# Performance work log

Hardware: AMD Instinct MI355X
Metric: run time of the kernel (lower is better)

Reference implementation:

```python
import jax, jax.numpy as jnp
import numpy as np

NV = 20000; NC = 20000; E = 500000
IN_SHAPE = 2; PE_DIM = 8; HID = 64; NL = 3
EPS = 1e-7  # GENConv message eps


def _lin(x, w, b):
    return x @ w + b


def _encode(x, pe, ew, eb, pw1, pb1, pw2, pb2):
    # relu(cat([Linear(x), 0.5*(pe_mlp(pe)+pe_mlp(-pe))], dim=1))
    def pe_mlp(p):
        return _lin(jax.nn.relu(_lin(p, pw1, pb1)), pw2, pb2)
    h = jnp.concatenate([_lin(x, ew, eb), 0.5 * (pe_mlp(pe) + pe_mlp(-pe))], axis=1)
    return jax.nn.relu(h)


def _genconv(x_src, x_dst, src, dst, ewt, lew, leb, w1, b1, w2, b2, n_dst):
    # GENConv(aggr='softmax', t=1, norm=None, msg_norm=False, edge_dim=1)
    msg = jax.nn.relu(x_src[src] + _lin(ewt, lew, leb)) + EPS  # [E, HID]
    m = jax.ops.segment_max(msg, dst, num_segments=n_dst)      # stable segment softmax
    ex = jnp.exp(msg - m[dst])
    s = jax.ops.segment_sum(ex, dst, num_segments=n_dst)
    agg = jax.ops.segment_sum(ex / (s[dst] + 1e-16) * msg, dst, num_segments=n_dst)
    out = agg + x_dst
    return _lin(jax.nn.relu(_lin(out, w1, b1)), w2, b2)  # MLP [hid -> 2hid -> hid]


def setup_inputs() -> dict:
    key = jax.random.key(0)
    ks = iter(jax.random.split(key, 64))
    d = {}
    d['x_vals'] = jax.random.normal(next(ks), (NV, IN_SHAPE), jnp.float32)
    d['x_cons'] = jax.random.normal(next(ks), (NC, IN_SHAPE), jnp.float32)
    d['pe_vals'] = jax.random.normal(next(ks), (NV, PE_DIM), jnp.float32)
    d['pe_cons'] = jax.random.normal(next(ks), (NC, PE_DIM), jnp.float32)
    d['edge_index_v2c'] = jnp.stack([
        jax.random.randint(next(ks), (E,), 0, NV),
        jax.random.randint(next(ks), (E,), 0, NC)])
    d['edge_index_c2v'] = jnp.stack([
        jax.random.randint(next(ks), (E,), 0, NC),
        jax.random.randint(next(ks), (E,), 0, NV)])
    d['edge_weight_v2c'] = jax.random.normal(next(ks), (E, 1), jnp.float32)
    d['edge_weight_c2v'] = jax.random.normal(next(ks), (E, 1), jnp.float32)
    def p(shape):
        return jax.random.normal(next(ks), shape, jnp.float32) * 0.05
    for k_ in ['vals', 'cons']:
        d[f'enc_{k_}_w'] = p((IN_SHAPE, HID // 2)); d[f'enc_{k_}_b'] = p((HID // 2,))
        d[f'pe_{k_}_w1'] = p((PE_DIM, HID)); d[f'pe_{k_}_b1'] = p((HID,))
        d[f'pe_{k_}_w2'] = p((HID, HID // 2)); d[f'pe_{k_}_b2'] = p((HID // 2,))
    for c in ['v2c', 'c2v']:
        d[f'{c}_edge_w'] = p((NL, 1, HID)); d[f'{c}_edge_b'] = p((NL, HID))
        d[f'{c}_w1'] = p((NL, HID, 2 * HID)); d[f'{c}_b1'] = p((NL, 2 * HID))
        d[f'{c}_w2'] = p((NL, 2 * HID, HID)); d[f'{c}_b2'] = p((NL, HID))
    for k_ in ['vals', 'cons']:
        d[f'pred_{k_}_w1'] = p((HID, HID)); d[f'pred_{k_}_b1'] = p((HID,))
        d[f'pred_{k_}_w2'] = p((HID, 1)); d[f'pred_{k_}_b2'] = p((1,))
    return d


def reference(x_vals, x_cons, pe_vals, pe_cons, edge_index_v2c, edge_index_c2v,
              edge_weight_v2c, edge_weight_c2v,
              enc_vals_w, enc_vals_b, pe_vals_w1, pe_vals_b1, pe_vals_w2, pe_vals_b2,
              enc_cons_w, enc_cons_b, pe_cons_w1, pe_cons_b1, pe_cons_w2, pe_cons_b2,
              v2c_edge_w, v2c_edge_b, v2c_w1, v2c_b1, v2c_w2, v2c_b2,
              c2v_edge_w, c2v_edge_b, c2v_w1, c2v_b1, c2v_w2, c2v_b2,
              pred_vals_w1, pred_vals_b1, pred_vals_w2, pred_vals_b2,
              pred_cons_w1, pred_cons_b1, pred_cons_w2, pred_cons_b2):
    vals = _encode(x_vals, pe_vals, enc_vals_w, enc_vals_b,
                   pe_vals_w1, pe_vals_b1, pe_vals_w2, pe_vals_b2)
    cons = _encode(x_cons, pe_cons, enc_cons_w, enc_cons_b,
                   pe_cons_w1, pe_cons_b1, pe_cons_w2, pe_cons_b2)
    hv, hc = [], []
    for i in range(NL):
        cons = _genconv(vals, cons, edge_index_v2c[0], edge_index_v2c[1],
                        edge_weight_v2c, v2c_edge_w[i], v2c_edge_b[i],
                        v2c_w1[i], v2c_b1[i], v2c_w2[i], v2c_b2[i], NC)
        vals = _genconv(cons, vals, edge_index_c2v[0], edge_index_c2v[1],
                        edge_weight_c2v, c2v_edge_w[i], c2v_edge_b[i],
                        c2v_w1[i], c2v_b1[i], c2v_w2[i], c2v_b2[i], NV)
        hc.append(cons); hv.append(vals)
    V = jnp.stack(hv)  # [NL, NV, HID]
    C = jnp.stack(hc)  # [NL, NC, HID]
    pv = _lin(jax.nn.relu(_lin(V, pred_vals_w1, pred_vals_b1)), pred_vals_w2, pred_vals_b2)
    pc = _lin(jax.nn.relu(_lin(C, pred_cons_w1, pred_cons_b1)), pred_cons_w2, pred_cons_b2)
    return pv[..., 0].T, pc[..., 0].T  # [NV, NL], [NC, NL]
```

## Files before the change

### kernel.cpp

```cpp
#include <hip/hip_runtime.h>
#include <hip/hip_fp16.h>

#define NVN 20000
#define NCN 20000
#define NE  500000
#define HID 64
#define NLAYER 3
#define TN 40
#define BSH 8
#define NB 79
#define CAPSH 14
#define CAP (1 << CAPSH)
#define NBCAP (NB * CAP)
#define P1E 2048
#define NTILES (NVN / TN)
#define SNAPL (NLAYER - 1)

__device__ __forceinline__ float relu_(float x) { return fmaxf(x, 0.0f); }

__global__ __launch_bounds__(256) void bininit_kernel(
    int* __restrict__ bincurA, int* __restrict__ bincurB)
{
    int t = threadIdx.x;
    if (t < NB) { bincurA[t] = t << CAPSH; bincurB[t] = t << CAPSH; }
}

__global__ __launch_bounds__(256) void scatter_p1_kernel(
    const int* __restrict__ eiA, const float* __restrict__ ewA,
    int* __restrict__ bincurA, int2* __restrict__ stageA,
    const int* __restrict__ eiB, const float* __restrict__ ewB,
    int* __restrict__ bincurB, int2* __restrict__ stageB)
{
    __shared__ int rnk[P1E];
    __shared__ int cnt[NB], base_[NB];
    int t = threadIdx.x;
    int e0 = blockIdx.x * P1E;

    for (int g = 0; g < 2; ++g) {
        const int* ei   = g ? eiB : eiA;
        const float* ew = g ? ewB : ewA;
        int* bincur     = g ? bincurB : bincurA;
        int2* stage     = g ? stageB : stageA;

        if (t < NB) cnt[t] = 0;
        __syncthreads();
        for (int i = t; i < P1E; i += 256) {
            int e = e0 + i;
            if (e < NE) {
                int d = ei[NE + e];
                rnk[i] = atomicAdd(&cnt[d >> BSH], 1);
            }
        }
        __syncthreads();
        if (t < NB && cnt[t] > 0) base_[t] = atomicAdd(&bincur[t], cnt[t]);
        __syncthreads();
        for (int i = t; i < P1E; i += 256) {
            int e = e0 + i;
            if (e < NE) {
                int s = ei[e], d = ei[NE + e];
                float w = ew[e];
                stage[base_[d >> BSH] + rnk[i]] =
                    make_int2((int)((unsigned)s | ((unsigned)d << 16)), __float_as_int(w));
            }
        }
        __syncthreads();
    }
}

__global__ __launch_bounds__(1024) void scatter_p2_kernel(
    const int* __restrict__ bincurA, const int2* __restrict__ stageA,
    int* __restrict__ rowptrA, int* __restrict__ rowendA, int2* __restrict__ pairA,
    const int* __restrict__ bincurB, const int2* __restrict__ stageB,
    int* __restrict__ rowptrB, int* __restrict__ rowendB, int2* __restrict__ pairB)
{
    __shared__ int deg[256], pfx[256], cur[256];
    int g = blockIdx.x / NB;
    int b = blockIdx.x % NB;
    const int* bincur  = g ? bincurB : bincurA;
    const int2* stage  = g ? stageB : stageA;
    int* rowptr        = g ? rowptrB : rowptrA;
    int* rowend        = g ? rowendB : rowendA;
    int2* pair         = g ? pairB : pairA;

    int d0 = b << BSH;
    int d1 = min(d0 + 256, NCN);
    int nd = d1 - d0;
    int t = threadIdx.x;
    int estart = b << CAPSH;
    int eend = bincur[b];

    if (t < 256) deg[t] = 0;
    __syncthreads();
    for (int e = estart + t; e < eend; e += 1024) {
        int dst = (int)((unsigned)stage[e].x >> 16);
        atomicAdd(&deg[dst - d0], 1);
    }
    __syncthreads();
    if (t < 256) pfx[t] = deg[t];
    __syncthreads();
    for (int off = 1; off < 256; off <<= 1) {
        int v = (t >= off && t < 256) ? pfx[t - off] : 0;
        __syncthreads();
        if (t < 256) pfx[t] += v;
        __syncthreads();
    }
    if (t < nd) {
        int ex = estart + pfx[t] - deg[t];
        rowptr[d0 + t] = ex;
        rowend[d0 + t] = estart + pfx[t];
        cur[t] = ex;
    }
    __syncthreads();
    for (int e = estart + t; e < eend; e += 1024) {
        int2 s = stage[e];
        unsigned u = (unsigned)s.x;
        int src = (int)(u & 0xFFFFu);
        int dst = (int)(u >> 16);
        int p = atomicAdd(&cur[dst - d0], 1);
        pair[p] = make_int2(src, s.y);
    }
}

__global__ __launch_bounds__(256) void encode2_kernel(
    const float* __restrict__ xv, const float* __restrict__ pev,
    const float* __restrict__ ewv, const float* __restrict__ ebv,
    const float* __restrict__ pw1v, const float* __restrict__ pb1v,
    const float* __restrict__ pw2v, const float* __restrict__ pb2v,
    const float* __restrict__ xc, const float* __restrict__ pec,
    const float* __restrict__ ewc, const float* __restrict__ ebc,
    const float* __restrict__ pw1c, const float* __restrict__ pb1c,
    const float* __restrict__ pw2c, const float* __restrict__ pb2c,
    float* __restrict__ outv, float* __restrict__ outc,
    __half* __restrict__ outv16, __half* __restrict__ outc16)
{
    __shared__ float sh[4][64];
    const int VB = (NVN + 3) / 4;
    int wave = threadIdx.x >> 6, lane = threadIdx.x & 63;
    int b = blockIdx.x;
    bool isC = (b >= VB);
    const float* x   = isC ? xc : xv;
    const float* pe  = isC ? pec : pev;
    const float* ew  = isC ? ewc : ewv;
    const float* eb  = isC ? ebc : ebv;
    const float* pw1 = isC ? pw1c : pw1v;
    const float* pb1 = isC ? pb1c : pb1v;
    const float* pw2 = isC ? pw2c : pw2v;
    const float* pb2 = isC ? pb2c : pb2v;
    float* out = isC ? outc : outv;
    __half* out16 = isC ? outc16 : outv16;
    int N = isC ? NCN : NVN;
    int n = (isC ? b - VB : b) * 4 + wave;
    if (n >= N) return;

    float accp = pb1[lane], accm = accp;
#pragma unroll
    for (int k = 0; k < 8; ++k) {
        float p = pe[n * 8 + k];
        float w = pw1[k * 64 + lane];
        accp += p * w;
        accm -= p * w;
    }
    float hs = 0.5f * (relu_(accp) + relu_(accm));
    float* my = sh[wave];
    my[lane] = hs;
    __builtin_amdgcn_wave_barrier();

    int col = lane & 31;
    float peo = pb2[col];
#pragma unroll
    for (int k = 0; k < 64; k += 4) {
        float4 hv = *(const float4*)(my + k);
        peo = fmaf(hv.x, pw2[(k + 0) * 32 + col], peo);
        peo = fmaf(hv.y, pw2[(k + 1) * 32 + col], peo);
        peo = fmaf(hv.z, pw2[(k + 2) * 32 + col], peo);
        peo = fmaf(hv.w, pw2[(k + 3) * 32 + col], peo);
    }
    float lino = x[n * 2 + 0] * ew[col] + x[n * 2 + 1] * ew[32 + col] + eb[col];
    float h = (lane < 32) ? lino : peo;
    float r = relu_(h);
    out[n * 64 + lane] = r;
    out16[n * 64 + lane] = __float2half(r);
}

__global__ __launch_bounds__(256, 8) void edge_agg_kernel(
    const __half* __restrict__ xsrc,
    const float* __restrict__ xdst,
    const int* __restrict__ rowptr,
    const int* __restrict__ rowend,
    const int2* __restrict__ pair,
    const float* __restrict__ lew,
    const float* __restrict__ leb,
    float* __restrict__ oa,
    int N)
{
    int wave = threadIdx.x >> 6, lane = threadIdx.x & 63;
    int n = blockIdx.x * 4 + wave;
    if (n >= N) return;

    int start = __builtin_amdgcn_readfirstlane(rowptr[n]);
    int end   = __builtin_amdgcn_readfirstlane(rowend[n]);
    float lw = lew[lane], lb = leb[lane];
    float xd = xdst[(size_t)n * 64 + lane];

    float den = 0.0f, num = 0.0f;
    int j = start;

    if (j + 8 <= end) {
        int2 pb[8];
#pragma unroll
        for (int c = 0; c < 8; ++c) pb[c] = pair[j + c];

        for (; j + 16 <= end; j += 8) {
            float xv[8];
#pragma unroll
            for (int c = 0; c < 8; ++c)
                xv[c] = __half2float(xsrc[(size_t)pb[c].x * 64 + lane]);
            int2 pn[8];
#pragma unroll
            for (int c = 0; c < 8; ++c) pn[c] = pair[j + 8 + c];
#pragma unroll
            for (int c = 0; c < 8; ++c) {
                float msg = relu_(fmaf(__int_as_float(pb[c].y), lw, xv[c] + lb)) + 1e-7f;
                float e = __expf(msg);
                den += e;
                num = fmaf(e, msg, num);
            }
#pragma unroll
            for (int c = 0; c < 8; ++c) pb[c] = pn[c];
        }
        {
            float xv[8];
#pragma unroll
            for (int c = 0; c < 8; ++c)
                xv[c] = __half2float(xsrc[(size_t)pb[c].x * 64 + lane]);
#pragma unroll
            for (int c = 0; c < 8; ++c) {
                float msg = relu_(fmaf(__int_as_float(pb[c].y), lw, xv[c] + lb)) + 1e-7f;
                float e = __expf(msg);
                den += e;
                num = fmaf(e, msg, num);
            }
            j += 8;
        }
    }
    for (; j < end; ++j) {
        int2 p = pair[j];
        float xv = __half2float(xsrc[(size_t)p.x * 64 + lane]);
        float msg = relu_(fmaf(__int_as_float(p.y), lw, xv + lb)) + 1e-7f;
        float e = __expf(msg);
        den += e;
        num = fmaf(e, msg, num);
    }

    oa[(size_t)n * 64 + lane] = num / (den + 1e-16f) + xd;
}

__global__ __launch_bounds__(256, 4) void mlp_kernel(
    const float* __restrict__ oa,
    float* __restrict__ feat,
    __half* __restrict__ feat16,
    float* __restrict__ snap,
    const float* __restrict__ w1,
    const float* __restrict__ b1,
    const float* __restrict__ w2,
    const float* __restrict__ b2,
    int N)
{
    __shared__ float act[TN][68];
    __shared__ float hid[TN][132];
    __shared__ float b1s[128];
    __shared__ float b2s[64];

    int tid = threadIdx.x;
    if (tid < 128) b1s[tid] = b1[tid];
    if (tid < 64) b2s[tid] = b2[tid];

    int o4 = (tid & 31) * 4;
    int o2 = (tid & 31) * 2;
    int n5 = (tid >> 5) * 5;
    __syncthreads();

    int ntiles = N / TN;
    for (int tile = blockIdx.x; tile < ntiles; tile += gridDim.x) {
        int base = tile * TN;
        {
            const float4* g4 = (const float4*)(oa + (size_t)base * 64);
            for (int i = tid; i < TN * 16; i += 256)
                *(float4*)&act[i >> 4][(i & 15) * 4] = g4[i];
        }
        __syncthreads();

        {
            float acc[5][4];
#pragma unroll
            for (int i = 0; i < 5; ++i)
#pragma unroll
                for (int q = 0; q < 4; ++q) acc[i][q] = b1s[o4 + q];
#pragma unroll 2
            for (int k = 0; k < 64; k += 4) {
                float4 a[5];
#pragma unroll
                for (int i = 0; i < 5; ++i) a[i] = *(const float4*)&act[n5 + i][k];
                float4 w0 = *(const float4*)&w1[(k + 0) * 128 + o4];
                float4 wq1 = *(const float4*)&w1[(k + 1) * 128 + o4];
                float4 wq2 = *(const float4*)&w1[(k + 2) * 128 + o4];
                float4 wq3 = *(const float4*)&w1[(k + 3) * 128 + o4];
#pragma unroll
                for (int i = 0; i < 5; ++i) {
                    acc[i][0] = fmaf(a[i].x, w0.x, acc[i][0]);
                    acc[i][1] = fmaf(a[i].x, w0.y, acc[i][1]);
                    acc[i][2] = fmaf(a[i].x, w0.z, acc[i][2]);
                    acc[i][3] = fmaf(a[i].x, w0.w, acc[i][3]);
                    acc[i][0] = fmaf(a[i].y, wq1.x, acc[i][0]);
                    acc[i][1] = fmaf(a[i].y, wq1.y, acc[i][1]);
                    acc[i][2] = fmaf(a[i].y, wq1.z, acc[i][2]);
                    acc[i][3] = fmaf(a[i].y, wq1.w, acc[i][3]);
                    acc[i][0] = fmaf(a[i].z, wq2.x, acc[i][0]);
                    acc[i][1] = fmaf(a[i].z, wq2.y, acc[i][1]);
                    acc[i][2] = fmaf(a[i].z, wq2.z, acc[i][2]);
                    acc[i][3] = fmaf(a[i].z, wq2.w, acc[i][3]);
                    acc[i][0] = fmaf(a[i].w, wq3.x, acc[i][0]);
                    acc[i][1] = fmaf(a[i].w, wq3.y, acc[i][1]);
                    acc[i][2] = fmaf(a[i].w, wq3.z, acc[i][2]);
                    acc[i][3] = fmaf(a[i].w, wq3.w, acc[i][3]);
                }
            }
#pragma unroll
            for (int i = 0; i < 5; ++i) {
                float4 h4 = make_float4(relu_(acc[i][0]), relu_(acc[i][1]),
                                        relu_(acc[i][2]), relu_(acc[i][3]));
                *(float4*)&hid[n5 + i][o4] = h4;
            }
        }
        __syncthreads();

        {
            float acc[5][2];
#pragma unroll
            for (int i = 0; i < 5; ++i) { acc[i][0] = b2s[o2]; acc[i][1] = b2s[o2 + 1]; }
#pragma unroll 2
            for (int k = 0; k < 128; k += 4) {
                float4 a[5];
#pragma unroll
                for (int i = 0; i < 5; ++i) a[i] = *(const float4*)&hid[n5 + i][k];
                float2 w0 = *(const float2*)&w2[(k + 0) * 64 + o2];
                float2 wq1 = *(const float2*)&w2[(k + 1) * 64 + o2];
                float2 wq2 = *(const float2*)&w2[(k + 2) * 64 + o2];
                float2 wq3 = *(const float2*)&w2[(k + 3) * 64 + o2];
#pragma unroll
                for (int i = 0; i < 5; ++i) {
                    acc[i][0] = fmaf(a[i].x, w0.x, acc[i][0]);
                    acc[i][1] = fmaf(a[i].x, w0.y, acc[i][1]);
                    acc[i][0] = fmaf(a[i].y, wq1.x, acc[i][0]);
                    acc[i][1] = fmaf(a[i].y, wq1.y, acc[i][1]);
                    acc[i][0] = fmaf(a[i].z, wq2.x, acc[i][0]);
                    acc[i][1] = fmaf(a[i].z, wq2.y, acc[i][1]);
                    acc[i][0] = fmaf(a[i].w, wq3.x, acc[i][0]);
                    acc[i][1] = fmaf(a[i].w, wq3.y, acc[i][1]);
                }
            }
#pragma unroll
            for (int i = 0; i < 5; ++i) {
                float2 r2 = make_float2(acc[i][0], acc[i][1]);
                size_t off = (size_t)(base + n5 + i) * 64 + o2;
                *(float2*)&feat[off] = r2;
                if (snap) *(float2*)&snap[off] = r2;
                *(__half2*)&feat16[off] = __floats2half2_rn(r2.x, r2.y);
            }
        }
        __syncthreads();
    }
}

__global__ __launch_bounds__(256, 4) void pred_kernel(
    const float* __restrict__ snap,
    const float* __restrict__ featv,
    const float* __restrict__ featc,
    const float* __restrict__ pv_w1, const float* __restrict__ pv_b1,
    const float* __restrict__ pv_w2, const float* __restrict__ pv_b2,
    const float* __restrict__ pc_w1, const float* __restrict__ pc_b1,
    const float* __restrict__ pc_w2, const float* __restrict__ pc_b2,
    float* __restrict__ out)
{
    __shared__ float act[TN][68];
    __shared__ float pb1s[64];
    __shared__ float pw2s[64];

    int bid = blockIdx.x;
    int side  = bid / (NLAYER * NTILES);
    int rem   = bid % (NLAYER * NTILES);
    int layer = rem / NTILES;
    int tile  = rem % NTILES;

    const float* pw1 = side ? pc_w1 : pv_w1;
    const float* pb1 = side ? pc_b1 : pv_b1;
    const float* pw2 = side ? pc_w2 : pv_w2;
    const float* pb2 = side ? pc_b2 : pv_b2;
    const float* src;
    if (layer == NLAYER - 1)
        src = side ? featc : featv;
    else
        src = snap + ((size_t)side * SNAPL + layer) * ((size_t)NVN * 64);
    float* outp = out + (size_t)side * NVN * NLAYER;

    int tid = threadIdx.x;
    if (tid < 64) { pb1s[tid] = pb1[tid]; pw2s[tid] = pw2[tid]; }
    float pb2v = pb2[0];

    int o2 = (tid & 31) * 2;
    int n5 = (tid >> 5) * 5;
    int base = tile * TN;

    {
        const float4* g4 = (const float4*)(src + (size_t)base * 64);
        for (int i = tid; i < TN * 16; i += 256)
            *(float4*)&act[i >> 4][(i & 15) * 4] = g4[i];
    }
    __syncthreads();

    float acc[5][2];
#pragma unroll
    for (int i = 0; i < 5; ++i) { acc[i][0] = pb1s[o2]; acc[i][1] = pb1s[o2 + 1]; }
#pragma unroll 2
    for (int k = 0; k < 64; k += 4) {
        float4 a[5];
#pragma unroll
        for (int i = 0; i < 5; ++i) a[i] = *(const float4*)&act[n5 + i][k];
        float2 w0 = *(const float2*)&pw1[(k + 0) * 64 + o2];
        float2 wq1 = *(const float2*)&pw1[(k + 1) * 64 + o2];
        float2 wq2 = *(const float2*)&pw1[(k + 2) * 64 + o2];
        float2 wq3 = *(const float2*)&pw1[(k + 3) * 64 + o2];
#pragma unroll
        for (int i = 0; i < 5; ++i) {
            acc[i][0] = fmaf(a[i].x, w0.x, acc[i][0]);
            acc[i][1] = fmaf(a[i].x, w0.y, acc[i][1]);
            acc[i][0] = fmaf(a[i].y, wq1.x, acc[i][0]);
            acc[i][1] = fmaf(a[i].y, wq1.y, acc[i][1]);
            acc[i][0] = fmaf(a[i].z, wq2.x, acc[i][0]);
            acc[i][1] = fmaf(a[i].z, wq2.y, acc[i][1]);
            acc[i][0] = fmaf(a[i].w, wq3.x, acc[i][0]);
            acc[i][1] = fmaf(a[i].w, wq3.y, acc[i][1]);
        }
    }
    float pw2a = pw2s[o2], pw2b = pw2s[o2 + 1];
    float ps[5];
#pragma unroll
    for (int i = 0; i < 5; ++i)
        ps[i] = relu_(acc[i][0]) * pw2a + relu_(acc[i][1]) * pw2b;
#pragma unroll
    for (int msk = 16; msk >= 1; msk >>= 1) {
#pragma unroll
        for (int i = 0; i < 5; ++i)
            ps[i] += __shfl_xor(ps[i], msk, 64);
    }
    if ((tid & 31) == 0) {
#pragma unroll
        for (int i = 0; i < 5; ++i)
            outp[(size_t)(base + n5 + i) * NLAYER + layer] = ps[i] + pb2v;
    }
}

extern "C" void kernel_launch(void* const* d_in, const int* in_sizes, int n_in,
                              void* d_out, int out_size, void* d_ws, size_t ws_size,
                              hipStream_t stream)
{
    const float* x_vals   = (const float*)d_in[0];
    const float* x_cons   = (const float*)d_in[1];
    const float* pe_vals  = (const float*)d_in[2];
    const float* pe_cons  = (const float*)d_in[3];
    const int*   ei_v2c   = (const int*)d_in[4];
    const int*   ei_c2v   = (const int*)d_in[5];
    const float* ew_v2c   = (const float*)d_in[6];
    const float* ew_c2v   = (const float*)d_in[7];
    const float* enc_vals_w = (const float*)d_in[8];
    const float* enc_vals_b = (const float*)d_in[9];
    const float* pe_vals_w1 = (const float*)d_in[10];
    const float* pe_vals_b1 = (const float*)d_in[11];
    const float* pe_vals_w2 = (const float*)d_in[12];
    const float* pe_vals_b2 = (const float*)d_in[13];
    const float* enc_cons_w = (const float*)d_in[14];
    const float* enc_cons_b = (const float*)d_in[15];
    const float* pe_cons_w1 = (const float*)d_in[16];
    const float* pe_cons_b1 = (const float*)d_in[17];
    const float* pe_cons_w2 = (const float*)d_in[18];
    const float* pe_cons_b2 = (const float*)d_in[19];
    const float* v2c_edge_w = (const float*)d_in[20];
    const float* v2c_edge_b = (const float*)d_in[21];
    const float* v2c_w1     = (const float*)d_in[22];
    const float* v2c_b1     = (const float*)d_in[23];
    const float* v2c_w2     = (const float*)d_in[24];
    const float* v2c_b2     = (const float*)d_in[25];
    const float* c2v_edge_w = (const float*)d_in[26];
    const float* c2v_edge_b = (const float*)d_in[27];
    const float* c2v_w1     = (const float*)d_in[28];
    const float* c2v_b1     = (const float*)d_in[29];
    const float* c2v_w2     = (const float*)d_in[30];
    const float* c2v_b2     = (const float*)d_in[31];
    const float* pred_vals_w1 = (const float*)d_in[32];
    const float* pred_vals_b1 = (const float*)d_in[33];
    const float* pred_vals_w2 = (const float*)d_in[34];
    const float* pred_vals_b2 = (const float*)d_in[35];
    const float* pred_cons_w1 = (const float*)d_in[36];
    const float* pred_cons_b1 = (const float*)d_in[37];
    const float* pred_cons_w2 = (const float*)d_in[38];
    const float* pred_cons_b2 = (const float*)d_in[39];

    float* out = (float*)d_out;

    const size_t NF = (size_t)NVN * 64;

    float* ws     = (float*)d_ws;
    float* feat_v = ws;
    float* feat_c = feat_v + NF;
    float* oa     = feat_c + NF;
    int2* v2c_pair  = (int2*)(oa + NF);
    int2* c2v_pair  = v2c_pair + NBCAP;
    int2* v2c_stage = c2v_pair + NBCAP;
    int2* c2v_stage = v2c_stage + NBCAP;
    float* snap = (float*)v2c_stage;
    __half* feat16_v = (__half*)(c2v_stage + NBCAP);
    __half* feat16_c = feat16_v + NF;
    int* ip = (int*)(feat16_c + NF);
    int* v2c_bincur  = ip; ip += NB;
    int* c2v_bincur  = ip; ip += NB;
    int* v2c_rowptr  = ip; ip += NCN;
    int* v2c_rowend  = ip; ip += NCN;
    int* c2v_rowptr  = ip; ip += NVN;
    int* c2v_rowend  = ip; ip += NVN;

    const int p1b = (NE + P1E - 1) / P1E;

    bininit_kernel<<<1, 256, 0, stream>>>(v2c_bincur, c2v_bincur);
    scatter_p1_kernel<<<p1b, 256, 0, stream>>>(
        ei_v2c, ew_v2c, v2c_bincur, v2c_stage,
        ei_c2v, ew_c2v, c2v_bincur, c2v_stage);
    scatter_p2_kernel<<<2 * NB, 1024, 0, stream>>>(
        v2c_bincur, v2c_stage, v2c_rowptr, v2c_rowend, v2c_pair,
        c2v_bincur, c2v_stage, c2v_rowptr, c2v_rowend, c2v_pair);

    encode2_kernel<<<(NVN + 3) / 4 + (NCN + 3) / 4, 256, 0, stream>>>(
        x_vals, pe_vals, enc_vals_w, enc_vals_b,
        pe_vals_w1, pe_vals_b1, pe_vals_w2, pe_vals_b2,
        x_cons, pe_cons, enc_cons_w, enc_cons_b,
        pe_cons_w1, pe_cons_b1, pe_cons_w2, pe_cons_b2,
        feat_v, feat_c, feat16_v, feat16_c);

    for (int i = 0; i < NLAYER; ++i) {
        float* snap_c = (i < SNAPL) ? snap + ((size_t)SNAPL + i) * NF : nullptr;
        float* snap_v = (i < SNAPL) ? snap + (size_t)i * NF : nullptr;
        edge_agg_kernel<<<(NCN + 3) / 4, 256, 0, stream>>>(
            feat16_v, feat_c, v2c_rowptr, v2c_rowend, v2c_pair,
            v2c_edge_w + (size_t)i * HID, v2c_edge_b + (size_t)i * HID,
            oa, NCN);
        mlp_kernel<<<NCN / TN, 256, 0, stream>>>(
            oa, feat_c, feat16_c, snap_c,
            v2c_w1 + (size_t)i * 8192, v2c_b1 + (size_t)i * 128,
            v2c_w2 + (size_t)i * 8192, v2c_b2 + (size_t)i * 64,
            NCN);
        edge_agg_kernel<<<(NVN + 3) / 4, 256, 0, stream>>>(
            feat16_c, feat_v, c2v_rowptr, c2v_rowend, c2v_pair,
            c2v_edge_w + (size_t)i * HID, c2v_edge_b + (size_t)i * HID,
            oa, NVN);
        mlp_kernel<<<NVN / TN, 256, 0, stream>>>(
            oa, feat_v, feat16_v, snap_v,
            c2v_w1 + (size_t)i * 8192, c2v_b1 + (size_t)i * 128,
            c2v_w2 + (size_t)i * 8192, c2v_b2 + (size_t)i * 64,
            NVN);
    }

    pred_kernel<<<2 * NLAYER * NTILES, 256, 0, stream>>>(
        snap, feat_v, feat_c,
        pred_vals_w1, pred_vals_b1, pred_vals_w2, pred_vals_b2,
        pred_cons_w1, pred_cons_b1, pred_cons_w2, pred_cons_b2,
        out);
}
```

Before: 423.5 us.

## Process two edges per wave using half2 feature loads in edge aggregation

The edge aggregation kernel now splits each 64-lane wave into two half-waves. Each half-wave handles alternate edges, and each lane loads a packed half2 covering two feature channels, so one wave processes two edges per step. The partial softmax numerators and denominators are combined with a cross-half shuffle before the write. This aims to double the edges in flight and widen the gather loads, at the cost of extra registers, a shuffle reduction, and tail handling for odd edge counts.

```diff
diff --git a/kernel.cpp b/kernel.cpp
--- a/kernel.cpp
+++ b/kernel.cpp
@@ -199,60 +199,85 @@
 
     int start = __builtin_amdgcn_readfirstlane(rowptr[n]);
     int end   = __builtin_amdgcn_readfirstlane(rowend[n]);
-    float lw = lew[lane], lb = leb[lane];
-    float xd = xdst[(size_t)n * 64 + lane];
-
-    float den = 0.0f, num = 0.0f;
+    int g  = lane >> 5;
+    int d  = lane & 31;
+    const unsigned* xs2 = (const unsigned*)xsrc;
+    float lw0 = lew[d * 2], lw1 = lew[d * 2 + 1];
+    float lb0 = leb[d * 2], lb1 = leb[d * 2 + 1];
+    float2 xd2 = ((const float2*)xdst)[(size_t)n * 32 + d];
+
+    float den0 = 0.0f, den1 = 0.0f, num0 = 0.0f, num1 = 0.0f;
     int j = start;
 
-    if (j + 8 <= end) {
+#define EDGE2(P, U) { \
+        __half2 h2 = *(const __half2*)&(U); \
+        float2 xf = __half22float2(h2); \
+        float w_ = __int_as_float((P).y); \
+        float m0 = relu_(fmaf(w_, lw0, xf.x + lb0)) + 1e-7f; \
+        float m1 = relu_(fmaf(w_, lw1, xf.y + lb1)) + 1e-7f; \
+        float e0 = __expf(m0), e1 = __expf(m1); \
+        den0 += e0; num0 = fmaf(e0, m0, num0); \
+        den1 += e1; num1 = fmaf(e1, m1, num1); }
+
+    if (j + 16 <= end) {
         int2 pb[8];
 #pragma unroll
-        for (int c = 0; c < 8; ++c) pb[c] = pair[j + c];
-
-        for (; j + 16 <= end; j += 8) {
-            float xv[8];
+        for (int c = 0; c < 8; ++c) pb[c] = pair[j + 2 * c + g];
+
+        for (; j + 32 <= end; j += 16) {
+            unsigned xv[8];
 #pragma unroll
             for (int c = 0; c < 8; ++c)
-                xv[c] = __half2float(xsrc[(size_t)pb[c].x * 64 + lane]);
+                xv[c] = xs2[(size_t)pb[c].x * 32 + d];
             int2 pn[8];
 #pragma unroll
-            for (int c = 0; c < 8; ++c) pn[c] = pair[j + 8 + c];
-#pragma unroll
-            for (int c = 0; c < 8; ++c) {
-                float msg = relu_(fmaf(__int_as_float(pb[c].y), lw, xv[c] + lb)) + 1e-7f;
-                float e = __expf(msg);
-                den += e;
-                num = fmaf(e, msg, num);
-            }
+            for (int c = 0; c < 8; ++c) pn[c] = pair[j + 16 + 2 * c + g];
+#pragma unroll
+            for (int c = 0; c < 8; ++c) EDGE2(pb[c], xv[c]);
 #pragma unroll
             for (int c = 0; c < 8; ++c) pb[c] = pn[c];
         }
         {
-            float xv[8];
+            unsigned xv[8];
 #pragma unroll
             for (int c = 0; c < 8; ++c)
-                xv[c] = __half2float(xsrc[(size_t)pb[c].x * 64 + lane]);
-#pragma unroll
-            for (int c = 0; c < 8; ++c) {
-                float msg = relu_(fmaf(__int_as_float(pb[c].y), lw, xv[c] + lb)) + 1e-7f;
-                float e = __expf(msg);
-                den += e;
-                num = fmaf(e, msg, num);
-            }
-            j += 8;
-        }
-    }
-    for (; j < end; ++j) {
+                xv[c] = xs2[(size_t)pb[c].x * 32 + d];
+#pragma unroll
+            for (int c = 0; c < 8; ++c) EDGE2(pb[c], xv[c]);
+            j += 16;
+        }
+    }
+    for (; j + 2 <= end; j += 2) {
+        int2 p = pair[j + g];
+        unsigned u = xs2[(size_t)p.x * 32 + d];
+        EDGE2(p, u);
+    }
+    if (j < end) {
         int2 p = pair[j];
-        float xv = __half2float(xsrc[(size_t)p.x * 64 + lane]);
-        float msg = relu_(fmaf(__int_as_float(p.y), lw, xv + lb)) + 1e-7f;
-        float e = __expf(msg);
-        den += e;
-        num = fmaf(e, msg, num);
-    }
-
-    oa[(size_t)n * 64 + lane] = num / (den + 1e-16f) + xd;
+        unsigned u = xs2[(size_t)p.x * 32 + d];
+        __half2 h2 = *(const __half2*)&u;
+        float2 xf = __half22float2(h2);
+        float w_ = __int_as_float(p.y);
+        float m0 = relu_(fmaf(w_, lw0, xf.x + lb0)) + 1e-7f;
+        float m1 = relu_(fmaf(w_, lw1, xf.y + lb1)) + 1e-7f;
+        float e0 = (g == 0) ? __expf(m0) : 0.0f;
+        float e1 = (g == 0) ? __expf(m1) : 0.0f;
+        den0 += e0; num0 = fmaf(e0, m0, num0);
+        den1 += e1; num1 = fmaf(e1, m1, num1);
+    }
+#undef EDGE2
+
+    den0 += __shfl_xor(den0, 32, 64);
+    den1 += __shfl_xor(den1, 32, 64);
+    num0 += __shfl_xor(num0, 32, 64);
+    num1 += __shfl_xor(num1, 32, 64);
+
+    if (lane < 32) {
+        float2 r;
+        r.x = num0 / (den0 + 1e-16f) + xd2.x;
+        r.y = num1 / (den1 + 1e-16f) + xd2.y;
+        ((float2*)oa)[(size_t)n * 32 + d] = r;
+    }
 }
 
 __global__ __launch_bounds__(256, 4) void mlp_kernel(
```

Result: slower. 441.6 us (+4.3%).
